# Kernel tuning notes

Hardware: AMD Instinct MI355X
Metric: run time of the kernel (lower is better)

The kernel has to match this reference:

```python
import jax, jax.numpy as jnp
import numpy as np

B, T_H, N, F_P = 16, 24, 256, 6
H, PRED_LEN, F_W = 64, 12, 4


def _build_static(coords):
    # haversine distance matrix -> gaussian kernel -> threshold (epsilon=0.5)
    lon, lat = coords[:, 0], coords[:, 1]
    dlon = lon[None, :] - lon[:, None]
    dlat = lat[None, :] - lat[:, None]
    a = (np.sin(np.radians(dlat / 2)) ** 2
         + np.cos(np.radians(lat[:, None])) * np.cos(np.radians(lat[None, :]))
         * np.sin(np.radians(dlon / 2)) ** 2)
    dist = 2.0 * 6371.0 * np.arcsin(np.sqrt(np.clip(a, 0.0, None)))
    std = dist.flatten().std()
    adj = np.exp(-np.square(dist / std))
    adj[adj < 0.5] = 0.0
    return adj.astype(np.float32)


def setup_inputs() -> dict:
    key = jax.random.key(0)
    ks = jax.random.split(key, 16)
    rng = np.random.default_rng(0)
    coords_np = np.stack([116.0 + rng.uniform(-1.0, 1.0, N),
                          40.0 + rng.uniform(-1.0, 1.0, N)], axis=1).astype(np.float32)
    s = 0.05
    scale_w = jnp.asarray([1.0, 360.0, 10.0, 1.0], jnp.float32)  # [_, dir(deg), speed, _]
    return {
        "history_pollution": jax.random.normal(ks[0], (B, T_H, N, F_P), jnp.float32),
        "history_weather": jax.random.uniform(ks[1], (B, T_H, F_W), jnp.float32) * scale_w,
        "static_adj": jnp.asarray(_build_static(coords_np)),
        "coords": jnp.asarray(coords_np),
        "w_gc1": jax.random.normal(ks[2], (H, F_P), jnp.float32) * s,
        "b_gc1": jax.random.normal(ks[3], (H,), jnp.float32) * s,
        "w_gc2": jax.random.normal(ks[4], (H, H), jnp.float32) * s,
        "b_gc2": jax.random.normal(ks[5], (H,), jnp.float32) * s,
        "w_ih": jax.random.normal(ks[6], (3 * H, H), jnp.float32) * s,
        "w_hh": jax.random.normal(ks[7], (3 * H, H), jnp.float32) * s,
        "b_ih": jax.random.normal(ks[8], (3 * H,), jnp.float32) * s,
        "b_hh": jax.random.normal(ks[9], (3 * H,), jnp.float32) * s,
        "w_m1": jax.random.normal(ks[10], (32, H), jnp.float32) * s,
        "b_m1": jax.random.normal(ks[11], (32,), jnp.float32) * s,
        "w_m2": jax.random.normal(ks[12], (F_P, 32), jnp.float32) * s,
        "b_m2": jax.random.normal(ks[13], (F_P,), jnp.float32) * s,
    }


def _forward(history_pollution, history_weather, static_adj, coords,
             w_gc1, b_gc1, w_gc2, b_gc2, w_ih, w_hh, b_ih, b_hh,
             w_m1, b_m1, w_m2, b_m2):
    Bs, Th, Ns, Fp = history_pollution.shape
    dt = history_pollution.dtype
    eye = jnp.eye(Ns, dtype=dt)
    # station pair angles: vecs[i,j] = coords[j] - coords[i]
    vecs = coords[None, :, :] - coords[:, None, :]
    ang = jnp.arctan2(vecs[..., 1], vecs[..., 0])  # [N,N]

    def gconv(x, adj, w, b):
        wt = adj + eye[None]                         # [B,N,N]
        d = 1.0 / (jnp.sqrt(wt.sum(-1)) + 1e-6)      # [B,N]
        norm = d[:, :, None] * wt * d[:, None, :]    # D^-1/2 W D^-1/2
        return jnp.einsum('bij,bjf->bif', norm, x) @ w.T + b

    def gcb(x, w_out, w_in):
        h1 = jax.nn.relu(gconv(x, w_out, w_gc1, b_gc1))
        return jax.nn.relu(gconv(h1, w_in, w_gc2, b_gc2))

    def gru(h, x):                                   # h,x: [B*N,H]
        gi = x @ w_ih.T + b_ih
        gh = h @ w_hh.T + b_hh
        i_r, i_z, i_n = jnp.split(gi, 3, axis=-1)
        h_r, h_z, h_n = jnp.split(gh, 3, axis=-1)
        r = jax.nn.sigmoid(i_r + h_r)
        z = jax.nn.sigmoid(i_z + h_z)
        n = jnp.tanh(i_n + r * h_n)
        return (1.0 - z) * n + z * h

    def mlp(x):
        return jax.nn.relu(x @ w_m1.T + b_m1) @ w_m2.T + b_m2

    def enc_step(carry, xs):
        h, _ = carry
        x_t, spd, wd = xs                            # [B,N,F],[B],[B]
        rad = jnp.deg2rad(wd)
        w_dyn = jnp.maximum(spd[:, None, None] * jnp.cos(ang[None] - rad[:, None, None]), 0.0)
        w_out = static_adj[None] * w_dyn             # [B,N,N]
        sf = gcb(x_t, w_out, jnp.swapaxes(w_out, 1, 2))
        h = gru(h, sf.reshape(Bs * Ns, -1))
        return (h, w_out), None

    h0 = jnp.zeros((Bs * Ns, w_hh.shape[1]), dt)
    xs = (jnp.moveaxis(history_pollution, 1, 0),      # [T,B,N,F]
          history_weather[:, :, 2].T,                 # wind speed [T,B]
          history_weather[:, :, 1].T)                 # wind dir   [T,B]
    (h, last_w_out), _ = jax.lax.scan(enc_step, (h0, jnp.zeros((Bs, Ns, Ns), dt)), xs)
    last_w_in = jnp.swapaxes(last_w_out, 1, 2)

    dec0 = mlp(h.reshape(Bs, Ns, -1))

    def dec_step(carry, _):
        h_c, x = carry
        sf = gcb(x, last_w_out, last_w_in)
        h_c = gru(h_c, sf.reshape(Bs * Ns, -1))
        pred = mlp(h_c.reshape(Bs, Ns, -1))
        return (h_c, pred), pred

    _, preds = jax.lax.scan(dec_step, (h, dec0), None, length=PRED_LEN)
    return jnp.moveaxis(preds, 0, 1)                  # [B, pred_len, N, F_P]


def reference(history_pollution, history_weather, static_adj, coords,
              w_gc1, b_gc1, w_gc2, b_gc2, w_ih, w_hh, b_ih, b_hh,
              w_m1, b_m1, w_m2, b_m2):
    return _forward(history_pollution, history_weather, static_adj, coords,
                    w_gc1, b_gc1, w_gc2, b_gc2, w_ih, w_hh, b_ih, b_hh,
                    w_m1, b_m1, w_m2, b_m2)
```

## Files before the change

### kernel.cpp

```cpp
#include <hip/hip_runtime.h>
#include <math.h>

#define Bsz 16
#define Tt 24
#define Nn 256
#define Fp 6
#define Hh 64
#define PredL 12
#define Fw 4
#define G3 192
#define M1 32
#define DEG2RAD 0.017453292519943295f
#define IDX2(t, b) ((t) * Bsz + (b))

__global__ __launch_bounds__(256) void k_prep_ang(
    const float* __restrict__ coords, const float* __restrict__ adj,
    float* __restrict__ Ac, float* __restrict__ As) {
  int i = blockIdx.x;
  int j = threadIdx.x;
  float dx = coords[2 * j]     - coords[2 * i];
  float dy = coords[2 * j + 1] - coords[2 * i + 1];
  float ang = atan2f(dy, dx);
  float a = adj[i * Nn + j];
  Ac[i * Nn + j] = a * cosf(ang);
  As[i * Nn + j] = a * sinf(ang);
}

__global__ __launch_bounds__(256) void k_transpose_weights(
    const float* __restrict__ wgc2, const float* __restrict__ wih,
    const float* __restrict__ whh,  const float* __restrict__ wm1,
    const float* __restrict__ wm2,
    float* __restrict__ wgc2T, float* __restrict__ wihT, float* __restrict__ whhT,
    float* __restrict__ wm1T, float* __restrict__ wm2T) {
  int tid = threadIdx.x;
  for (int idx = tid; idx < Hh * Hh; idx += 256) {
    int g = idx / Hh, k = idx % Hh;
    wgc2T[k * Hh + g] = wgc2[g * Hh + k];
  }
  for (int idx = tid; idx < G3 * Hh; idx += 256) {
    int g = idx / Hh, k = idx % Hh;
    wihT[k * G3 + g] = wih[g * Hh + k];
    whhT[k * G3 + g] = whh[g * Hh + k];
  }
  for (int idx = tid; idx < M1 * Hh; idx += 256) {
    int m = idx / Hh, k = idx % Hh;
    wm1T[k * M1 + m] = wm1[m * Hh + k];
  }
  for (int idx = tid; idx < Fp * M1; idx += 256) {
    int f = idx / M1, m = idx % M1;
    wm2T[m * Fp + f] = wm2[f * M1 + m];
  }
}

__global__ __launch_bounds__(256) void k_deg(
    const float* __restrict__ hw, const float* __restrict__ Ac,
    const float* __restrict__ As,
    float* __restrict__ dbuf, float* __restrict__ ebuf) {
  int q  = blockIdx.x & 3;
  int tb = blockIdx.x >> 2;
  int t = tb / Bsz, b = tb % Bsz;
  float spd = hw[(b * Tt + t) * Fw + 2];
  float rad = hw[(b * Tt + t) * Fw + 1] * DEG2RAD;
  float cr = cosf(rad), sr = sinf(rad);
  int w = threadIdx.x >> 6, lane = threadIdx.x & 63;
  for (int m = 0; m < 16; ++m) {
    int i = q * 64 + w * 16 + m;
    float rs = 0.f, cs = 0.f;
#pragma unroll
    for (int c = 0; c < 4; ++c) {
      int j = lane + 64 * c;
      float val = spd * (Ac[i * Nn + j] * cr + As[i * Nn + j] * sr);
      rs += fmaxf(val, 0.f);
      cs += (j == i) ? fmaxf(val, 0.f) : fmaxf(-val, 0.f);
    }
#pragma unroll
    for (int off = 32; off; off >>= 1) {
      rs += __shfl_xor(rs, off);
      cs += __shfl_xor(cs, off);
    }
    if (lane == 0) {
      dbuf[IDX2(t, b) * Nn + i] = 1.f / (sqrtf(rs + 1.f) + 1e-6f);
      ebuf[IDX2(t, b) * Nn + i] = 1.f / (sqrtf(cs + 1.f) + 1e-6f);
    }
  }
}

__global__ __launch_bounds__(256) void k_gconv1_enc(
    const float* __restrict__ hp, const float* __restrict__ hw,
    const float* __restrict__ Ac, const float* __restrict__ As,
    const float* __restrict__ dbuf,
    const float* __restrict__ wgc1, const float* __restrict__ bgc1,
    float* __restrict__ h1_all) {
  __shared__ float d_lds[Nn];
  __shared__ float x_lds[Nn * Fp];
  int ig = blockIdx.x & 15;
  int tb = blockIdx.x >> 4;
  int t = tb / Bsz, b = tb % Bsz;
  int i0 = ig * 16;
  int tid = threadIdx.x, w = tid >> 6, lane = tid & 63;
  float spd = hw[(b * Tt + t) * Fw + 2];
  float rad = hw[(b * Tt + t) * Fw + 1] * DEG2RAD;
  float cr = cosf(rad), sr = sinf(rad);
  d_lds[tid] = dbuf[IDX2(t, b) * Nn + tid];
  const float* xsrc = hp + (long)(b * Tt + t) * Nn * Fp;
#pragma unroll
  for (int c = 0; c < 6; ++c) x_lds[tid + 256 * c] = xsrc[tid + 256 * c];
  __syncthreads();
#pragma unroll
  for (int rr = 0; rr < 4; ++rr) {
    int i = i0 + w * 4 + rr;
    float acc[Fp] = {0.f, 0.f, 0.f, 0.f, 0.f, 0.f};
#pragma unroll
    for (int c = 0; c < 4; ++c) {
      int j = lane + 64 * c;
      float val = spd * (Ac[i * Nn + j] * cr + As[i * Nn + j] * sr);
      float wt = fmaxf(val, 0.f) * d_lds[j];
#pragma unroll
      for (int f = 0; f < Fp; ++f) acc[f] += wt * x_lds[j * Fp + f];
    }
#pragma unroll
    for (int f = 0; f < Fp; ++f) {
#pragma unroll
      for (int off = 32; off; off >>= 1) acc[f] += __shfl_xor(acc[f], off);
    }
    float di = d_lds[i];
    float y[Fp];
#pragma unroll
    for (int f = 0; f < Fp; ++f) y[f] = di * (acc[f] + di * x_lds[i * Fp + f]);
    float hv = bgc1[lane];
#pragma unroll
    for (int f = 0; f < Fp; ++f) hv += wgc1[lane * Fp + f] * y[f];
    h1_all[((long)IDX2(t, b) * Nn + i) * Hh + lane] = fmaxf(hv, 0.f);
  }
}

__global__ __launch_bounds__(256) void k_gconv2_enc(
    const float* __restrict__ hw, const float* __restrict__ Ac,
    const float* __restrict__ As, const float* __restrict__ ebuf,
    const float* __restrict__ h1_all,
    const float* __restrict__ wgc2T, const float* __restrict__ bgc2,
    float* __restrict__ sf_all) {
  __shared__ float e_lds[Nn];
  __shared__ __align__(16) float wvT[Nn * 20];
  __shared__ float red[4][16][Hh];
  __shared__ float y2[16][Hh];
  int ig = blockIdx.x & 15;
  int tb = blockIdx.x >> 4;
  int t = tb / Bsz, b = tb % Bsz;
  int i0 = ig * 16;
  int tid = threadIdx.x, w = tid >> 6, lane = tid & 63;
  float spd = hw[(b * Tt + t) * Fw + 2];
  float rad = hw[(b * Tt + t) * Fw + 1] * DEG2RAD;
  float cr = cosf(rad), sr = sinf(rad);
  e_lds[tid] = ebuf[IDX2(t, b) * Nn + tid];
  __syncthreads();
  float ej = e_lds[tid];
#pragma unroll
  for (int r = 0; r < 16; ++r) {
    int i = i0 + r;
    int j = tid;
    float val = spd * (Ac[i * Nn + j] * cr + As[i * Nn + j] * sr);
    float wt = (j == i) ? (fmaxf(val, 0.f) * ej + ej) : (fmaxf(-val, 0.f) * ej);
    wvT[j * 20 + r] = wt;
  }
  __syncthreads();
  float acc[16];
#pragma unroll
  for (int r = 0; r < 16; ++r) acc[r] = 0.f;
  const float* h1b = h1_all + (long)IDX2(t, b) * Nn * Hh;
#pragma unroll 4
  for (int jj = 0; jj < 64; ++jj) {
    int j = w * 64 + jj;
    float hv = h1b[j * Hh + lane];
    const float4* wp = (const float4*)(wvT + j * 20);
    float4 w0 = wp[0], w1 = wp[1], w2 = wp[2], w3 = wp[3];
    acc[0] += w0.x * hv; acc[1] += w0.y * hv; acc[2] += w0.z * hv; acc[3] += w0.w * hv;
    acc[4] += w1.x * hv; acc[5] += w1.y * hv; acc[6] += w1.z * hv; acc[7] += w1.w * hv;
    acc[8] += w2.x * hv; acc[9] += w2.y * hv; acc[10] += w2.z * hv; acc[11] += w2.w * hv;
    acc[12] += w3.x * hv; acc[13] += w3.y * hv; acc[14] += w3.z * hv; acc[15] += w3.w * hv;
  }
#pragma unroll
  for (int r = 0; r < 16; ++r) red[w][r][lane] = acc[r];
  __syncthreads();
#pragma unroll
  for (int rr = 0; rr < 4; ++rr) {
    int r = w * 4 + rr;
    float v = red[0][r][lane] + red[1][r][lane] + red[2][r][lane] + red[3][r][lane];
    y2[r][lane] = v * e_lds[i0 + r];
  }
  float a0 = bgc2[lane], a1 = a0, a2 = a0, a3 = a0;
  for (int k = 0; k < Hh; ++k) {
    float wk = wgc2T[k * Hh + lane];
    a0 += wk * y2[w * 4 + 0][k];
    a1 += wk * y2[w * 4 + 1][k];
    a2 += wk * y2[w * 4 + 2][k];
    a3 += wk * y2[w * 4 + 3][k];
  }
  long base = ((long)IDX2(t, b) * Nn + i0 + w * 4) * Hh + lane;
  sf_all[base + 0 * Hh] = fmaxf(a0, 0.f);
  sf_all[base + 1 * Hh] = fmaxf(a1, 0.f);
  sf_all[base + 2 * Hh] = fmaxf(a2, 0.f);
  sf_all[base + 3 * Hh] = fmaxf(a3, 0.f);
}

__global__ __launch_bounds__(256) void k_gru_scan(
    const float* __restrict__ sf_all,
    const float* __restrict__ wihT, const float* __restrict__ whhT,
    const float* __restrict__ bih, const float* __restrict__ bhh,
    float* __restrict__ hstate) {
  __shared__ float wih_s[Hh * G3];
  __shared__ float whh_s[Hh * G3];
  int b = blockIdx.x >> 4;
  int i0 = (blockIdx.x & 15) * 16;
  int tid = threadIdx.x, w = tid >> 6, lane = tid & 63;
  for (int idx = tid; idx < Hh * G3; idx += 256) {
    wih_s[idx] = wihT[idx];
    whh_s[idx] = whhT[idx];
  }
  __syncthreads();
  float bi_r = bih[lane], bi_z = bih[64 + lane], bi_n = bih[128 + lane];
  float bh_r = bhh[lane], bh_z = bhh[64 + lane], bh_n = bhh[128 + lane];
  float h_reg[4] = {0.f, 0.f, 0.f, 0.f};
  for (int t = 0; t < Tt; ++t) {
    float sf_reg[4];
#pragma unroll
    for (int rr = 0; rr < 4; ++rr)
      sf_reg[rr] = sf_all[((long)IDX2(t, b) * Nn + i0 + w * 4 + rr) * Hh + lane];
    float gir[4], giz[4], gin[4], ghr[4], ghz[4], ghn[4];
#pragma unroll
    for (int rr = 0; rr < 4; ++rr) {
      gir[rr] = bi_r; giz[rr] = bi_z; gin[rr] = bi_n;
      ghr[rr] = bh_r; ghz[rr] = bh_z; ghn[rr] = bh_n;
    }
#pragma unroll 4
    for (int k = 0; k < Hh; ++k) {
      float wir = wih_s[k * G3 + lane];
      float wiz = wih_s[k * G3 + 64 + lane];
      float win = wih_s[k * G3 + 128 + lane];
      float whr = whh_s[k * G3 + lane];
      float whz = whh_s[k * G3 + 64 + lane];
      float whn = whh_s[k * G3 + 128 + lane];
#pragma unroll
      for (int rr = 0; rr < 4; ++rr) {
        float sfk = __shfl(sf_reg[rr], k);
        float hk  = __shfl(h_reg[rr], k);
        gir[rr] += wir * sfk;
        giz[rr] += wiz * sfk;
        gin[rr] += win * sfk;
        ghr[rr] += whr * hk;
        ghz[rr] += whz * hk;
        ghn[rr] += whn * hk;
      }
    }
#pragma unroll
    for (int rr = 0; rr < 4; ++rr) {
      float rg = 1.f / (1.f + expf(-(gir[rr] + ghr[rr])));
      float zg = 1.f / (1.f + expf(-(giz[rr] + ghz[rr])));
      float ng = tanhf(gin[rr] + rg * ghn[rr]);
      h_reg[rr] = (1.f - zg) * ng + zg * h_reg[rr];
    }
  }
#pragma unroll
  for (int rr = 0; rr < 4; ++rr)
    hstate[((long)b * Nn + i0 + w * 4 + rr) * Hh + lane] = h_reg[rr];
}

__global__ __launch_bounds__(256) void k_norm_dec(
    const float* __restrict__ hw, const float* __restrict__ Ac,
    const float* __restrict__ As,
    const float* __restrict__ dbuf, const float* __restrict__ ebuf,
    float* __restrict__ A1d, float* __restrict__ A2d) {
  int b = blockIdx.x >> 8;
  int i = blockIdx.x & 255;
  int j = threadIdx.x;
  float spd = hw[(b * Tt + (Tt - 1)) * Fw + 2];
  float rad = hw[(b * Tt + (Tt - 1)) * Fw + 1] * DEG2RAD;
  float cr = cosf(rad), sr = sinf(rad);
  const float* drow = dbuf + IDX2(Tt - 1, b) * Nn;
  const float* erow = ebuf + IDX2(Tt - 1, b) * Nn;
  float val = spd * (Ac[i * Nn + j] * cr + As[i * Nn + j] * sr);
  float wout = fmaxf(val, 0.f);
  float win  = (j == i) ? wout : fmaxf(-val, 0.f);
  float dlt = (j == i) ? 1.f : 0.f;
  A1d[((long)b * Nn + i) * Nn + j] = drow[i] * (wout + dlt) * drow[j];
  A2d[((long)b * Nn + i) * Nn + j] = erow[i] * (win + dlt) * erow[j];
}

__global__ __launch_bounds__(256) void k_gconv1_dec(
    const float* __restrict__ xb, const float* __restrict__ A1d,
    const float* __restrict__ wgc1, const float* __restrict__ bgc1,
    float* __restrict__ h1d) {
  __shared__ float x_lds[Nn * Fp];
  int b = blockIdx.x >> 4;
  int i0 = (blockIdx.x & 15) * 16;
  int tid = threadIdx.x, w = tid >> 6, lane = tid & 63;
  const float* xsrc = xb + (long)b * Nn * Fp;
#pragma unroll
  for (int c = 0; c < 6; ++c) x_lds[tid + 256 * c] = xsrc[tid + 256 * c];
  __syncthreads();
#pragma unroll
  for (int rr = 0; rr < 4; ++rr) {
    int i = i0 + w * 4 + rr;
    const float* arow = A1d + ((long)b * Nn + i) * Nn;
    float acc[Fp] = {0.f, 0.f, 0.f, 0.f, 0.f, 0.f};
#pragma unroll
    for (int c = 0; c < 4; ++c) {
      int j = lane + 64 * c;
      float wt = arow[j];
#pragma unroll
      for (int f = 0; f < Fp; ++f) acc[f] += wt * x_lds[j * Fp + f];
    }
#pragma unroll
    for (int f = 0; f < Fp; ++f) {
#pragma unroll
      for (int off = 32; off; off >>= 1) acc[f] += __shfl_xor(acc[f], off);
    }
    float hv = bgc1[lane];
#pragma unroll
    for (int f = 0; f < Fp; ++f) hv += wgc1[lane * Fp + f] * acc[f];
    h1d[((long)b * Nn + i) * Hh + lane] = fmaxf(hv, 0.f);
  }
}

__global__ __launch_bounds__(256) void k_gconv2_gru_dec(
    const float* __restrict__ A2d, const float* __restrict__ h1d,
    const float* __restrict__ wgc2T, const float* __restrict__ bgc2,
    const float* __restrict__ wihT, const float* __restrict__ whhT,
    const float* __restrict__ bih, const float* __restrict__ bhh,
    float* __restrict__ hstate,
    const float* __restrict__ wm1T, const float* __restrict__ bm1,
    const float* __restrict__ wm2T, const float* __restrict__ bm2,
    float* __restrict__ outp, float* __restrict__ xnext, int p) {
  __shared__ __align__(16) float wvT[Nn * 20];
  __shared__ float red[4][16][Hh];
  __shared__ float y2[16][Hh];
  __shared__ float hn_lds[16][Hh];
  __shared__ float u_lds[16][M1];
  __shared__ float wih_s[Hh * G3];
  __shared__ float whh_s[Hh * G3];
  int b = blockIdx.x >> 4;
  int i0 = (blockIdx.x & 15) * 16;
  int tid = threadIdx.x, w = tid >> 6, lane = tid & 63;

  for (int idx = tid; idx < Hh * G3; idx += 256) {
    wih_s[idx] = wihT[idx];
    whh_s[idx] = whhT[idx];
  }
#pragma unroll
  for (int r = 0; r < 16; ++r)
    wvT[tid * 20 + r] = A2d[((long)b * Nn + i0 + r) * Nn + tid];
  float hp_reg[4];
#pragma unroll
  for (int rr = 0; rr < 4; ++rr)
    hp_reg[rr] = hstate[((long)b * Nn + i0 + w * 4 + rr) * Hh + lane];
  __syncthreads();

  float acc[16];
#pragma unroll
  for (int r = 0; r < 16; ++r) acc[r] = 0.f;
  const float* h1b = h1d + (long)b * Nn * Hh;
#pragma unroll 4
  for (int jj = 0; jj < 64; ++jj) {
    int j = w * 64 + jj;
    float hv = h1b[j * Hh + lane];
    const float4* wp = (const float4*)(wvT + j * 20);
    float4 w0 = wp[0], w1 = wp[1], w2 = wp[2], w3 = wp[3];
    acc[0] += w0.x * hv; acc[1] += w0.y * hv; acc[2] += w0.z * hv; acc[3] += w0.w * hv;
    acc[4] += w1.x * hv; acc[5] += w1.y * hv; acc[6] += w1.z * hv; acc[7] += w1.w * hv;
    acc[8] += w2.x * hv; acc[9] += w2.y * hv; acc[10] += w2.z * hv; acc[11] += w2.w * hv;
    acc[12] += w3.x * hv; acc[13] += w3.y * hv; acc[14] += w3.z * hv; acc[15] += w3.w * hv;
  }
#pragma unroll
  for (int r = 0; r < 16; ++r) red[w][r][lane] = acc[r];
  __syncthreads();
#pragma unroll
  for (int rr = 0; rr < 4; ++rr) {
    int r = w * 4 + rr;
    y2[r][lane] = red[0][r][lane] + red[1][r][lane] + red[2][r][lane] + red[3][r][lane];
  }
  float a0 = bgc2[lane], a1 = a0, a2 = a0, a3 = a0;
  for (int k = 0; k < Hh; ++k) {
    float wk = wgc2T[k * Hh + lane];
    a0 += wk * y2[w * 4 + 0][k];
    a1 += wk * y2[w * 4 + 1][k];
    a2 += wk * y2[w * 4 + 2][k];
    a3 += wk * y2[w * 4 + 3][k];
  }
  float sf_reg[4];
  sf_reg[0] = fmaxf(a0, 0.f);
  sf_reg[1] = fmaxf(a1, 0.f);
  sf_reg[2] = fmaxf(a2, 0.f);
  sf_reg[3] = fmaxf(a3, 0.f);

  float gir[4], giz[4], gin[4], ghr[4], ghz[4], ghn[4];
#pragma unroll
  for (int rr = 0; rr < 4; ++rr) {
    gir[rr] = bih[lane]; giz[rr] = bih[64 + lane]; gin[rr] = bih[128 + lane];
    ghr[rr] = bhh[lane]; ghz[rr] = bhh[64 + lane]; ghn[rr] = bhh[128 + lane];
  }
#pragma unroll 4
  for (int k = 0; k < Hh; ++k) {
    float wir = wih_s[k * G3 + lane];
    float wiz = wih_s[k * G3 + 64 + lane];
    float win = wih_s[k * G3 + 128 + lane];
    float whr = whh_s[k * G3 + lane];
    float whz = whh_s[k * G3 + 64 + lane];
    float whn = whh_s[k * G3 + 128 + lane];
#pragma unroll
    for (int rr = 0; rr < 4; ++rr) {
      float sfk = __shfl(sf_reg[rr], k);
      float hk  = __shfl(hp_reg[rr], k);
      gir[rr] += wir * sfk;
      giz[rr] += wiz * sfk;
      gin[rr] += win * sfk;
      ghr[rr] += whr * hk;
      ghz[rr] += whz * hk;
      ghn[rr] += whn * hk;
    }
  }
#pragma unroll
  for (int rr = 0; rr < 4; ++rr) {
    int row = w * 4 + rr;
    float rg = 1.f / (1.f + expf(-(gir[rr] + ghr[rr])));
    float zg = 1.f / (1.f + expf(-(giz[rr] + ghz[rr])));
    float ng = tanhf(gin[rr] + rg * ghn[rr]);
    float hn = (1.f - zg) * ng + zg * hp_reg[rr];
    hstate[((long)b * Nn + i0 + row) * Hh + lane] = hn;
    hn_lds[row][lane] = hn;
  }
  __syncthreads();
#pragma unroll
  for (int rep = 0; rep < 2; ++rep) {
    int idx = tid + rep * 256;
    int row = idx >> 5, m = idx & 31;
    float um = bm1[m];
    for (int k = 0; k < Hh; ++k) um += wm1T[k * M1 + m] * hn_lds[row][k];
    u_lds[row][m] = fmaxf(um, 0.f);
  }
  __syncthreads();
  if (tid < 16 * Fp) {
    int row = tid / Fp, f = tid % Fp;
    float pf = bm2[f];
#pragma unroll
    for (int m = 0; m < M1; ++m) pf += wm2T[m * Fp + f] * u_lds[row][m];
    int i = i0 + row;
    outp[(((long)b * PredL + p) * Nn + i) * Fp + f] = pf;
    xnext[((long)b * Nn + i) * Fp + f] = pf;
  }
}

__global__ __launch_bounds__(256) void k_dec0(
    const float* __restrict__ hstate,
    const float* __restrict__ wm1T, const float* __restrict__ bm1,
    const float* __restrict__ wm2T, const float* __restrict__ bm2,
    float* __restrict__ xnext) {
  const int RPB = 16;
  __shared__ float h_lds[RPB][Hh];
  __shared__ float u_lds[RPB][M1];
  int r0 = blockIdx.x * RPB;
  int tid = threadIdx.x;
#pragma unroll
  for (int c = 0; c < (RPB * Hh) / 256; ++c) {
    int idx = tid + c * 256;
    h_lds[idx >> 6][idx & 63] = hstate[(long)r0 * Hh + idx];
  }
  __syncthreads();
#pragma unroll
  for (int rep = 0; rep < 2; ++rep) {
    int idx = tid + rep * 256;
    int row = idx >> 5, m = idx & 31;
    float um = bm1[m];
    for (int k = 0; k < Hh; ++k) um += wm1T[k * M1 + m] * h_lds[row][k];
    u_lds[row][m] = fmaxf(um, 0.f);
  }
  __syncthreads();
  if (tid < RPB * Fp) {
    int row = tid / Fp, f = tid % Fp;
    float pf = bm2[f];
#pragma unroll
    for (int m = 0; m < M1; ++m) pf += wm2T[m * Fp + f] * u_lds[row][m];
    xnext[(r0 + row) * Fp + f] = pf;
  }
}

extern "C" void kernel_launch(void* const* d_in, const int* in_sizes, int n_in,
                              void* d_out, int out_size, void* d_ws, size_t ws_size,
                              hipStream_t stream) {
  const float* hp     = (const float*)d_in[0];
  const float* hw     = (const float*)d_in[1];
  const float* adj    = (const float*)d_in[2];
  const float* coords = (const float*)d_in[3];
  const float* wgc1   = (const float*)d_in[4];
  const float* bgc1   = (const float*)d_in[5];
  const float* wgc2   = (const float*)d_in[6];
  const float* bgc2   = (const float*)d_in[7];
  const float* wih    = (const float*)d_in[8];
  const float* whh    = (const float*)d_in[9];
  const float* bih    = (const float*)d_in[10];
  const float* bhh    = (const float*)d_in[11];
  const float* wm1    = (const float*)d_in[12];
  const float* bm1    = (const float*)d_in[13];
  const float* wm2    = (const float*)d_in[14];
  const float* bm2    = (const float*)d_in[15];
  float* out = (float*)d_out;

  float* w = (float*)d_ws;
  float* Ac     = w; w += Nn * Nn;
  float* As     = w; w += Nn * Nn;
  float* dbuf   = w; w += Tt * Bsz * Nn;
  float* ebuf   = w; w += Tt * Bsz * Nn;
  float* hstate = w; w += Bsz * Nn * Hh;
  float* h1_all = w; w += (long)Tt * Bsz * Nn * Hh;
  float* sf_all = w; w += (long)Tt * Bsz * Nn * Hh;
  float* h1d    = w; w += Bsz * Nn * Hh;
  float* xb     = w; w += Bsz * Nn * Fp;
  float* A1d    = w; w += Bsz * Nn * Nn;
  float* A2d    = w; w += Bsz * Nn * Nn;
  float* wgc2T  = w; w += Hh * Hh;
  float* wihT   = w; w += Hh * G3;
  float* whhT   = w; w += Hh * G3;
  float* wm1T   = w; w += Hh * M1;
  float* wm2T   = w; w += M1 * Fp;

  k_prep_ang<<<Nn, 256, 0, stream>>>(coords, adj, Ac, As);
  k_transpose_weights<<<1, 256, 0, stream>>>(wgc2, wih, whh, wm1, wm2,
                                             wgc2T, wihT, whhT, wm1T, wm2T);
  k_deg<<<Tt * Bsz * 4, 256, 0, stream>>>(hw, Ac, As, dbuf, ebuf);

  k_gconv1_enc<<<Tt * Bsz * 16, 256, 0, stream>>>(hp, hw, Ac, As, dbuf,
                                                  wgc1, bgc1, h1_all);
  k_gconv2_enc<<<Tt * Bsz * 16, 256, 0, stream>>>(hw, Ac, As, ebuf, h1_all,
                                                  wgc2T, bgc2, sf_all);
  k_gru_scan<<<Bsz * 16, 256, 0, stream>>>(sf_all, wihT, whhT, bih, bhh, hstate);

  k_norm_dec<<<Bsz * Nn, 256, 0, stream>>>(hw, Ac, As, dbuf, ebuf, A1d, A2d);
  k_dec0<<<Bsz * Nn / 16, 256, 0, stream>>>(hstate, wm1T, bm1, wm2T, bm2, xb);

  for (int p = 0; p < PredL; ++p) {
    k_gconv1_dec<<<Bsz * 16, 256, 0, stream>>>(xb, A1d, wgc1, bgc1, h1d);
    k_gconv2_gru_dec<<<Bsz * 16, 256, 0, stream>>>(
        A2d, h1d, wgc2T, bgc2, wihT, whhT, bih, bhh, hstate,
        wm1T, bm1, wm2T, bm2, out, xb, p);
  }
}
```

Baseline: 769.4 us.

## Fuse decoder steps into one kernel and repack GRU weights as float4

The two decoder kernels per prediction step become one kernel. Each block now recomputes the full first graph conv for its batch into shared memory, using a transposed adjacency matrix, and then runs gconv2, the GRU and the MLP. A ping-pong input buffer avoids a read/write race on the step's input features. The GRU weights are repacked into float4 gate triples read straight from global/L2 instead of being staged in large LDS arrays, and the encoder GRU scan uses 2 rows per wave with twice as many blocks. The trade-off is that each of the 16 blocks per batch redundantly reads the whole 256x256 adjacency and builds a 64 KB h1 tile in LDS, which may lower occupancy.

New measurement: 938.6 us. +22.0%, slower.

```diff
diff --git a/kernel.cpp b/kernel.cpp
--- a/kernel.cpp
+++ b/kernel.cpp
@@ -26,22 +26,17 @@
   As[i * Nn + j] = a * sinf(ang);
 }
 
-__global__ __launch_bounds__(256) void k_transpose_weights(
+__global__ __launch_bounds__(256) void k_prep_weights(
     const float* __restrict__ wgc2, const float* __restrict__ wih,
     const float* __restrict__ whh,  const float* __restrict__ wm1,
     const float* __restrict__ wm2,
-    float* __restrict__ wgc2T, float* __restrict__ wihT, float* __restrict__ whhT,
-    float* __restrict__ wm1T, float* __restrict__ wm2T) {
+    float* __restrict__ wgc2T, float* __restrict__ wm1T, float* __restrict__ wm2T,
+    float4* __restrict__ wihP, float4* __restrict__ whhP) {
   int tid = threadIdx.x;
   for (int idx = tid; idx < Hh * Hh; idx += 256) {
     int g = idx / Hh, k = idx % Hh;
     wgc2T[k * Hh + g] = wgc2[g * Hh + k];
   }
-  for (int idx = tid; idx < G3 * Hh; idx += 256) {
-    int g = idx / Hh, k = idx % Hh;
-    wihT[k * G3 + g] = wih[g * Hh + k];
-    whhT[k * G3 + g] = whh[g * Hh + k];
-  }
   for (int idx = tid; idx < M1 * Hh; idx += 256) {
     int m = idx / Hh, k = idx % Hh;
     wm1T[k * M1 + m] = wm1[m * Hh + k];
@@ -49,6 +44,15 @@
   for (int idx = tid; idx < Fp * M1; idx += 256) {
     int f = idx / M1, m = idx % M1;
     wm2T[m * Fp + f] = wm2[f * M1 + m];
+  }
+  for (int idx = tid; idx < Hh * 64; idx += 256) {
+    int k = idx >> 6, lane = idx & 63;
+    wihP[idx] = make_float4(wih[(0 * 64 + lane) * Hh + k],
+                            wih[(1 * 64 + lane) * Hh + k],
+                            wih[(2 * 64 + lane) * Hh + k], 0.f);
+    whhP[idx] = make_float4(whh[(0 * 64 + lane) * Hh + k],
+                            whh[(1 * 64 + lane) * Hh + k],
+                            whh[(2 * 64 + lane) * Hh + k], 0.f);
   }
 }
 
@@ -203,73 +207,74 @@
   sf_all[base + 3 * Hh] = fmaxf(a3, 0.f);
 }
 
-__global__ __launch_bounds__(256) void k_gru_scan(
+__global__ __launch_bounds__(256) void k_gru_scan3(
     const float* __restrict__ sf_all,
-    const float* __restrict__ wihT, const float* __restrict__ whhT,
+    const float4* __restrict__ wihP, const float4* __restrict__ whhP,
     const float* __restrict__ bih, const float* __restrict__ bhh,
     float* __restrict__ hstate) {
-  __shared__ float wih_s[Hh * G3];
-  __shared__ float whh_s[Hh * G3];
-  int b = blockIdx.x >> 4;
-  int i0 = (blockIdx.x & 15) * 16;
+  __shared__ float sf_s[8][Hh];
+  __shared__ float h_s[8][Hh];
+  int b = blockIdx.x >> 5;
+  int i0 = (blockIdx.x & 31) * 8;
   int tid = threadIdx.x, w = tid >> 6, lane = tid & 63;
-  for (int idx = tid; idx < Hh * G3; idx += 256) {
-    wih_s[idx] = wihT[idx];
-    whh_s[idx] = whhT[idx];
-  }
-  __syncthreads();
   float bi_r = bih[lane], bi_z = bih[64 + lane], bi_n = bih[128 + lane];
   float bh_r = bhh[lane], bh_z = bhh[64 + lane], bh_n = bhh[128 + lane];
-  float h_reg[4] = {0.f, 0.f, 0.f, 0.f};
+  float h_reg[2] = {0.f, 0.f};
+#pragma unroll
+  for (int rr = 0; rr < 2; ++rr) h_s[w * 2 + rr][lane] = 0.f;
+
   for (int t = 0; t < Tt; ++t) {
-    float sf_reg[4];
-#pragma unroll
-    for (int rr = 0; rr < 4; ++rr)
-      sf_reg[rr] = sf_all[((long)IDX2(t, b) * Nn + i0 + w * 4 + rr) * Hh + lane];
-    float gir[4], giz[4], gin[4], ghr[4], ghz[4], ghn[4];
-#pragma unroll
-    for (int rr = 0; rr < 4; ++rr) {
+#pragma unroll
+    for (int rr = 0; rr < 2; ++rr)
+      sf_s[w * 2 + rr][lane] =
+          sf_all[((long)IDX2(t, b) * Nn + i0 + w * 2 + rr) * Hh + lane];
+    float gir[2], giz[2], gin[2], ghr[2], ghz[2], ghn[2];
+#pragma unroll
+    for (int rr = 0; rr < 2; ++rr) {
       gir[rr] = bi_r; giz[rr] = bi_z; gin[rr] = bi_n;
       ghr[rr] = bh_r; ghz[rr] = bh_z; ghn[rr] = bh_n;
     }
 #pragma unroll 4
-    for (int k = 0; k < Hh; ++k) {
-      float wir = wih_s[k * G3 + lane];
-      float wiz = wih_s[k * G3 + 64 + lane];
-      float win = wih_s[k * G3 + 128 + lane];
-      float whr = whh_s[k * G3 + lane];
-      float whz = whh_s[k * G3 + 64 + lane];
-      float whn = whh_s[k * G3 + 128 + lane];
-#pragma unroll
-      for (int rr = 0; rr < 4; ++rr) {
-        float sfk = __shfl(sf_reg[rr], k);
-        float hk  = __shfl(h_reg[rr], k);
-        gir[rr] += wir * sfk;
-        giz[rr] += wiz * sfk;
-        gin[rr] += win * sfk;
-        ghr[rr] += whr * hk;
-        ghz[rr] += whz * hk;
-        ghn[rr] += whn * hk;
+    for (int kb = 0; kb < 16; ++kb) {
+      int k0 = kb * 4;
+      float4 wi[4], wh[4];
+#pragma unroll
+      for (int q = 0; q < 4; ++q) {
+        wi[q] = wihP[(k0 + q) * 64 + lane];
+        wh[q] = whhP[(k0 + q) * 64 + lane];
       }
-    }
-#pragma unroll
-    for (int rr = 0; rr < 4; ++rr) {
+#pragma unroll
+      for (int rr = 0; rr < 2; ++rr) {
+        const float4 s4 = *(const float4*)&sf_s[w * 2 + rr][k0];
+        const float4 h4 = *(const float4*)&h_s[w * 2 + rr][k0];
+        gir[rr] += s4.x * wi[0].x + s4.y * wi[1].x + s4.z * wi[2].x + s4.w * wi[3].x;
+        giz[rr] += s4.x * wi[0].y + s4.y * wi[1].y + s4.z * wi[2].y + s4.w * wi[3].y;
+        gin[rr] += s4.x * wi[0].z + s4.y * wi[1].z + s4.z * wi[2].z + s4.w * wi[3].z;
+        ghr[rr] += h4.x * wh[0].x + h4.y * wh[1].x + h4.z * wh[2].x + h4.w * wh[3].x;
+        ghz[rr] += h4.x * wh[0].y + h4.y * wh[1].y + h4.z * wh[2].y + h4.w * wh[3].y;
+        ghn[rr] += h4.x * wh[0].z + h4.y * wh[1].z + h4.z * wh[2].z + h4.w * wh[3].z;
+      }
+    }
+#pragma unroll
+    for (int rr = 0; rr < 2; ++rr) {
       float rg = 1.f / (1.f + expf(-(gir[rr] + ghr[rr])));
       float zg = 1.f / (1.f + expf(-(giz[rr] + ghz[rr])));
       float ng = tanhf(gin[rr] + rg * ghn[rr]);
-      h_reg[rr] = (1.f - zg) * ng + zg * h_reg[rr];
-    }
-  }
-#pragma unroll
-  for (int rr = 0; rr < 4; ++rr)
-    hstate[((long)b * Nn + i0 + w * 4 + rr) * Hh + lane] = h_reg[rr];
+      float hn = (1.f - zg) * ng + zg * h_reg[rr];
+      h_reg[rr] = hn;
+      h_s[w * 2 + rr][lane] = hn;
+    }
+  }
+#pragma unroll
+  for (int rr = 0; rr < 2; ++rr)
+    hstate[((long)b * Nn + i0 + w * 2 + rr) * Hh + lane] = h_reg[rr];
 }
 
 __global__ __launch_bounds__(256) void k_norm_dec(
     const float* __restrict__ hw, const float* __restrict__ Ac,
     const float* __restrict__ As,
     const float* __restrict__ dbuf, const float* __restrict__ ebuf,
-    float* __restrict__ A1d, float* __restrict__ A2d) {
+    float* __restrict__ AT, float* __restrict__ A2d) {
   int b = blockIdx.x >> 8;
   int i = blockIdx.x & 255;
   int j = threadIdx.x;
@@ -279,174 +284,10 @@
   const float* drow = dbuf + IDX2(Tt - 1, b) * Nn;
   const float* erow = ebuf + IDX2(Tt - 1, b) * Nn;
   float val = spd * (Ac[i * Nn + j] * cr + As[i * Nn + j] * sr);
-  float wout = fmaxf(val, 0.f);
-  float win  = (j == i) ? wout : fmaxf(-val, 0.f);
   float dlt = (j == i) ? 1.f : 0.f;
-  A1d[((long)b * Nn + i) * Nn + j] = drow[i] * (wout + dlt) * drow[j];
-  A2d[((long)b * Nn + i) * Nn + j] = erow[i] * (win + dlt) * erow[j];
-}
-
-__global__ __launch_bounds__(256) void k_gconv1_dec(
-    const float* __restrict__ xb, const float* __restrict__ A1d,
-    const float* __restrict__ wgc1, const float* __restrict__ bgc1,
-    float* __restrict__ h1d) {
-  __shared__ float x_lds[Nn * Fp];
-  int b = blockIdx.x >> 4;
-  int i0 = (blockIdx.x & 15) * 16;
-  int tid = threadIdx.x, w = tid >> 6, lane = tid & 63;
-  const float* xsrc = xb + (long)b * Nn * Fp;
-#pragma unroll
-  for (int c = 0; c < 6; ++c) x_lds[tid + 256 * c] = xsrc[tid + 256 * c];
-  __syncthreads();
-#pragma unroll
-  for (int rr = 0; rr < 4; ++rr) {
-    int i = i0 + w * 4 + rr;
-    const float* arow = A1d + ((long)b * Nn + i) * Nn;
-    float acc[Fp] = {0.f, 0.f, 0.f, 0.f, 0.f, 0.f};
-#pragma unroll
-    for (int c = 0; c < 4; ++c) {
-      int j = lane + 64 * c;
-      float wt = arow[j];
-#pragma unroll
-      for (int f = 0; f < Fp; ++f) acc[f] += wt * x_lds[j * Fp + f];
-    }
-#pragma unroll
-    for (int f = 0; f < Fp; ++f) {
-#pragma unroll
-      for (int off = 32; off; off >>= 1) acc[f] += __shfl_xor(acc[f], off);
-    }
-    float hv = bgc1[lane];
-#pragma unroll
-    for (int f = 0; f < Fp; ++f) hv += wgc1[lane * Fp + f] * acc[f];
-    h1d[((long)b * Nn + i) * Hh + lane] = fmaxf(hv, 0.f);
-  }
-}
-
-__global__ __launch_bounds__(256) void k_gconv2_gru_dec(
-    const float* __restrict__ A2d, const float* __restrict__ h1d,
-    const float* __restrict__ wgc2T, const float* __restrict__ bgc2,
-    const float* __restrict__ wihT, const float* __restrict__ whhT,
-    const float* __restrict__ bih, const float* __restrict__ bhh,
-    float* __restrict__ hstate,
-    const float* __restrict__ wm1T, const float* __restrict__ bm1,
-    const float* __restrict__ wm2T, const float* __restrict__ bm2,
-    float* __restrict__ outp, float* __restrict__ xnext, int p) {
-  __shared__ __align__(16) float wvT[Nn * 20];
-  __shared__ float red[4][16][Hh];
-  __shared__ float y2[16][Hh];
-  __shared__ float hn_lds[16][Hh];
-  __shared__ float u_lds[16][M1];
-  __shared__ float wih_s[Hh * G3];
-  __shared__ float whh_s[Hh * G3];
-  int b = blockIdx.x >> 4;
-  int i0 = (blockIdx.x & 15) * 16;
-  int tid = threadIdx.x, w = tid >> 6, lane = tid & 63;
-
-  for (int idx = tid; idx < Hh * G3; idx += 256) {
-    wih_s[idx] = wihT[idx];
-    whh_s[idx] = whhT[idx];
-  }
-#pragma unroll
-  for (int r = 0; r < 16; ++r)
-    wvT[tid * 20 + r] = A2d[((long)b * Nn + i0 + r) * Nn + tid];
-  float hp_reg[4];
-#pragma unroll
-  for (int rr = 0; rr < 4; ++rr)
-    hp_reg[rr] = hstate[((long)b * Nn + i0 + w * 4 + rr) * Hh + lane];
-  __syncthreads();
-
-  float acc[16];
-#pragma unroll
-  for (int r = 0; r < 16; ++r) acc[r] = 0.f;
-  const float* h1b = h1d + (long)b * Nn * Hh;
-#pragma unroll 4
-  for (int jj = 0; jj < 64; ++jj) {
-    int j = w * 64 + jj;
-    float hv = h1b[j * Hh + lane];
-    const float4* wp = (const float4*)(wvT + j * 20);
-    float4 w0 = wp[0], w1 = wp[1], w2 = wp[2], w3 = wp[3];
-    acc[0] += w0.x * hv; acc[1] += w0.y * hv; acc[2] += w0.z * hv; acc[3] += w0.w * hv;
-    acc[4] += w1.x * hv; acc[5] += w1.y * hv; acc[6] += w1.z * hv; acc[7] += w1.w * hv;
-    acc[8] += w2.x * hv; acc[9] += w2.y * hv; acc[10] += w2.z * hv; acc[11] += w2.w * hv;
-    acc[12] += w3.x * hv; acc[13] += w3.y * hv; acc[14] += w3.z * hv; acc[15] += w3.w * hv;
-  }
-#pragma unroll
-  for (int r = 0; r < 16; ++r) red[w][r][lane] = acc[r];
-  __syncthreads();
-#pragma unroll
-  for (int rr = 0; rr < 4; ++rr) {
-    int r = w * 4 + rr;
-    y2[r][lane] = red[0][r][lane] + red[1][r][lane] + red[2][r][lane] + red[3][r][lane];
-  }
-  float a0 = bgc2[lane], a1 = a0, a2 = a0, a3 = a0;
-  for (int k = 0; k < Hh; ++k) {
-    float wk = wgc2T[k * Hh + lane];
-    a0 += wk * y2[w * 4 + 0][k];
-    a1 += wk * y2[w * 4 + 1][k];
-    a2 += wk * y2[w * 4 + 2][k];
-    a3 += wk * y2[w * 4 + 3][k];
-  }
-  float sf_reg[4];
-  sf_reg[0] = fmaxf(a0, 0.f);
-  sf_reg[1] = fmaxf(a1, 0.f);
-  sf_reg[2] = fmaxf(a2, 0.f);
-  sf_reg[3] = fmaxf(a3, 0.f);
-
-  float gir[4], giz[4], gin[4], ghr[4], ghz[4], ghn[4];
-#pragma unroll
-  for (int rr = 0; rr < 4; ++rr) {
-    gir[rr] = bih[lane]; giz[rr] = bih[64 + lane]; gin[rr] = bih[128 + lane];
-    ghr[rr] = bhh[lane]; ghz[rr] = bhh[64 + lane]; ghn[rr] = bhh[128 + lane];
-  }
-#pragma unroll 4
-  for (int k = 0; k < Hh; ++k) {
-    float wir = wih_s[k * G3 + lane];
-    float wiz = wih_s[k * G3 + 64 + lane];
-    float win = wih_s[k * G3 + 128 + lane];
-    float whr = whh_s[k * G3 + lane];
-    float whz = whh_s[k * G3 + 64 + lane];
-    float whn = whh_s[k * G3 + 128 + lane];
-#pragma unroll
-    for (int rr = 0; rr < 4; ++rr) {
-      float sfk = __shfl(sf_reg[rr], k);
-      float hk  = __shfl(hp_reg[rr], k);
-      gir[rr] += wir * sfk;
-      giz[rr] += wiz * sfk;
-      gin[rr] += win * sfk;
-      ghr[rr] += whr * hk;
-      ghz[rr] += whz * hk;
-      ghn[rr] += whn * hk;
-    }
-  }
-#pragma unroll
-  for (int rr = 0; rr < 4; ++rr) {
-    int row = w * 4 + rr;
-    float rg = 1.f / (1.f + expf(-(gir[rr] + ghr[rr])));
-    float zg = 1.f / (1.f + expf(-(giz[rr] + ghz[rr])));
-    float ng = tanhf(gin[rr] + rg * ghn[rr]);
-    float hn = (1.f - zg) * ng + zg * hp_reg[rr];
-    hstate[((long)b * Nn + i0 + row) * Hh + lane] = hn;
-    hn_lds[row][lane] = hn;
-  }
-  __syncthreads();
-#pragma unroll
-  for (int rep = 0; rep < 2; ++rep) {
-    int idx = tid + rep * 256;
-    int row = idx >> 5, m = idx & 31;
-    float um = bm1[m];
-    for (int k = 0; k < Hh; ++k) um += wm1T[k * M1 + m] * hn_lds[row][k];
-    u_lds[row][m] = fmaxf(um, 0.f);
-  }
-  __syncthreads();
-  if (tid < 16 * Fp) {
-    int row = tid / Fp, f = tid % Fp;
-    float pf = bm2[f];
-#pragma unroll
-    for (int m = 0; m < M1; ++m) pf += wm2T[m * Fp + f] * u_lds[row][m];
-    int i = i0 + row;
-    outp[(((long)b * PredL + p) * Nn + i) * Fp + f] = pf;
-    xnext[((long)b * Nn + i) * Fp + f] = pf;
-  }
+  float wtji = (j == i) ? fmaxf(val, 0.f) : fmaxf(-val, 0.f);
+  AT[((long)b * Nn + i) * Nn + j]  = drow[j] * (wtji + dlt) * drow[i];
+  A2d[((long)b * Nn + i) * Nn + j] = erow[i] * (wtji + dlt) * erow[j];
 }
 
 __global__ __launch_bounds__(256) void k_dec0(
@@ -480,6 +321,179 @@
 #pragma unroll
     for (int m = 0; m < M1; ++m) pf += wm2T[m * Fp + f] * u_lds[row][m];
     xnext[(r0 + row) * Fp + f] = pf;
+  }
+}
+
+__global__ __launch_bounds__(256) void k_dec_step(
+    const float* __restrict__ AT, const float* __restrict__ A2d,
+    const float* __restrict__ xb_in, float* __restrict__ hstate,
+    const float4* __restrict__ wihP, const float4* __restrict__ whhP,
+    const float* __restrict__ wgc2T, const float* __restrict__ wgc1,
+    const float* __restrict__ bgc1, const float* __restrict__ bgc2,
+    const float* __restrict__ bih, const float* __restrict__ bhh,
+    const float* __restrict__ wm1T, const float* __restrict__ bm1,
+    const float* __restrict__ wm2T, const float* __restrict__ bm2,
+    float* __restrict__ outp, float* __restrict__ xb_out, int p) {
+  __shared__ float h1_s[Nn * Hh];
+  __shared__ __align__(16) float wvT[Nn * 20];
+  __shared__ __align__(16) float scr[4096];
+  __shared__ float y2[16][Hh];
+  __shared__ float sf_s[16][Hh];
+  __shared__ float h_s[16][Hh];
+
+  int b = blockIdx.x >> 4;
+  int i0 = (blockIdx.x & 15) * 16;
+  int tid = threadIdx.x, w = tid >> 6, lane = tid & 63;
+
+  for (int idx = tid; idx < Nn * Fp; idx += 256) {
+    int m = idx / Fp, f = idx % Fp;
+    scr[m * 8 + f] = xb_in[(long)b * Nn * Fp + idx];
+  }
+#pragma unroll
+  for (int r = 0; r < 16; ++r)
+    wvT[tid * 20 + r] = A2d[((long)b * Nn + i0 + r) * Nn + tid];
+  float hp_reg[4];
+#pragma unroll
+  for (int rr = 0; rr < 4; ++rr) {
+    hp_reg[rr] = hstate[((long)b * Nn + i0 + w * 4 + rr) * Hh + lane];
+    h_s[w * 4 + rr][lane] = hp_reg[rr];
+  }
+  float bi_r = bih[lane], bi_z = bih[64 + lane], bi_n = bih[128 + lane];
+  float bh_r = bhh[lane], bh_z = bhh[64 + lane], bh_n = bhh[128 + lane];
+  float wgc1r[Fp];
+#pragma unroll
+  for (int f = 0; f < Fp; ++f) wgc1r[f] = wgc1[lane * Fp + f];
+  float bgc1v = bgc1[lane], bgc2v = bgc2[lane];
+  __syncthreads();
+
+  {
+    float a0 = 0.f, a1 = 0.f, a2 = 0.f, a3 = 0.f, a4 = 0.f, a5 = 0.f;
+    const float* atb = AT + (long)b * Nn * Nn;
+#pragma unroll 4
+    for (int m = 0; m < Nn; ++m) {
+      float av = atb[m * Nn + tid];
+      float4 xlo = *(const float4*)&scr[m * 8];
+      float4 xhi = *(const float4*)&scr[m * 8 + 4];
+      a0 += av * xlo.x; a1 += av * xlo.y; a2 += av * xlo.z;
+      a3 += av * xlo.w; a4 += av * xhi.x; a5 += av * xhi.y;
+    }
+    __syncthreads();
+    scr[2048 + tid * 8 + 0] = a0; scr[2048 + tid * 8 + 1] = a1;
+    scr[2048 + tid * 8 + 2] = a2; scr[2048 + tid * 8 + 3] = a3;
+    scr[2048 + tid * 8 + 4] = a4; scr[2048 + tid * 8 + 5] = a5;
+  }
+  __syncthreads();
+
+#pragma unroll 4
+  for (int jj = 0; jj < 64; ++jj) {
+    int j = w * 64 + jj;
+    float4 ylo = *(const float4*)&scr[2048 + j * 8];
+    float4 yhi = *(const float4*)&scr[2048 + j * 8 + 4];
+    float hv = bgc1v + wgc1r[0] * ylo.x + wgc1r[1] * ylo.y + wgc1r[2] * ylo.z +
+               wgc1r[3] * ylo.w + wgc1r[4] * yhi.x + wgc1r[5] * yhi.y;
+    h1_s[j * Hh + lane] = fmaxf(hv, 0.f);
+  }
+  __syncthreads();
+
+  float acc[16];
+#pragma unroll
+  for (int r = 0; r < 16; ++r) acc[r] = 0.f;
+#pragma unroll 4
+  for (int jj = 0; jj < 64; ++jj) {
+    int j = w * 64 + jj;
+    float hv = h1_s[j * Hh + lane];
+    const float4* wp = (const float4*)(wvT + j * 20);
+    float4 w0 = wp[0], w1 = wp[1], w2 = wp[2], w3 = wp[3];
+    acc[0] += w0.x * hv; acc[1] += w0.y * hv; acc[2] += w0.z * hv; acc[3] += w0.w * hv;
+    acc[4] += w1.x * hv; acc[5] += w1.y * hv; acc[6] += w1.z * hv; acc[7] += w1.w * hv;
+    acc[8] += w2.x * hv; acc[9] += w2.y * hv; acc[10] += w2.z * hv; acc[11] += w2.w * hv;
+    acc[12] += w3.x * hv; acc[13] += w3.y * hv; acc[14] += w3.z * hv; acc[15] += w3.w * hv;
+  }
+  __syncthreads();
+#pragma unroll
+  for (int r = 0; r < 16; ++r) scr[w * 1024 + r * 64 + lane] = acc[r];
+  __syncthreads();
+#pragma unroll
+  for (int rr = 0; rr < 4; ++rr) {
+    int r = w * 4 + rr;
+    y2[r][lane] = scr[r * 64 + lane] + scr[1024 + r * 64 + lane] +
+                  scr[2048 + r * 64 + lane] + scr[3072 + r * 64 + lane];
+  }
+  {
+    float a0 = bgc2v, a1 = a0, a2 = a0, a3 = a0;
+    for (int k = 0; k < Hh; ++k) {
+      float wk = wgc2T[k * Hh + lane];
+      a0 += wk * y2[w * 4 + 0][k];
+      a1 += wk * y2[w * 4 + 1][k];
+      a2 += wk * y2[w * 4 + 2][k];
+      a3 += wk * y2[w * 4 + 3][k];
+    }
+    sf_s[w * 4 + 0][lane] = fmaxf(a0, 0.f);
+    sf_s[w * 4 + 1][lane] = fmaxf(a1, 0.f);
+    sf_s[w * 4 + 2][lane] = fmaxf(a2, 0.f);
+    sf_s[w * 4 + 3][lane] = fmaxf(a3, 0.f);
+  }
+
+  float hn_reg[4];
+  {
+    float gir[4], giz[4], gin[4], ghr[4], ghz[4], ghn[4];
+#pragma unroll
+    for (int rr = 0; rr < 4; ++rr) {
+      gir[rr] = bi_r; giz[rr] = bi_z; gin[rr] = bi_n;
+      ghr[rr] = bh_r; ghz[rr] = bh_z; ghn[rr] = bh_n;
+    }
+#pragma unroll 4
+    for (int kb = 0; kb < 16; ++kb) {
+      int k0 = kb * 4;
+      float4 wi[4], wh[4];
+#pragma unroll
+      for (int q = 0; q < 4; ++q) {
+        wi[q] = wihP[(k0 + q) * 64 + lane];
+        wh[q] = whhP[(k0 + q) * 64 + lane];
+      }
+#pragma unroll
+      for (int rr = 0; rr < 4; ++rr) {
+        const float4 s4 = *(const float4*)&sf_s[w * 4 + rr][k0];
+        const float4 h4 = *(const float4*)&h_s[w * 4 + rr][k0];
+        gir[rr] += s4.x * wi[0].x + s4.y * wi[1].x + s4.z * wi[2].x + s4.w * wi[3].x;
+        giz[rr] += s4.x * wi[0].y + s4.y * wi[1].y + s4.z * wi[2].y + s4.w * wi[3].y;
+        gin[rr] += s4.x * wi[0].z + s4.y * wi[1].z + s4.z * wi[2].z + s4.w * wi[3].z;
+        ghr[rr] += h4.x * wh[0].x + h4.y * wh[1].x + h4.z * wh[2].x + h4.w * wh[3].x;
+        ghz[rr] += h4.x * wh[0].y + h4.y * wh[1].y + h4.z * wh[2].y + h4.w * wh[3].y;
+        ghn[rr] += h4.x * wh[0].z + h4.y * wh[1].z + h4.z * wh[2].z + h4.w * wh[3].z;
+      }
+    }
+#pragma unroll
+    for (int rr = 0; rr < 4; ++rr) {
+      float rg = 1.f / (1.f + expf(-(gir[rr] + ghr[rr])));
+      float zg = 1.f / (1.f + expf(-(giz[rr] + ghz[rr])));
+      float ng = tanhf(gin[rr] + rg * ghn[rr]);
+      hn_reg[rr] = (1.f - zg) * ng + zg * hp_reg[rr];
+      hstate[((long)b * Nn + i0 + w * 4 + rr) * Hh + lane] = hn_reg[rr];
+    }
+  }
+
+  __syncthreads();
+#pragma unroll
+  for (int rr = 0; rr < 4; ++rr) scr[(w * 4 + rr) * 64 + lane] = hn_reg[rr];
+  __syncthreads();
+#pragma unroll
+  for (int rep = 0; rep < 2; ++rep) {
+    int idx = tid + rep * 256;
+    int row = idx >> 5, m = idx & 31;
+    float um = bm1[m];
+    for (int k = 0; k < Hh; ++k) um += wm1T[k * M1 + m] * scr[row * 64 + k];
+    scr[1024 + row * M1 + m] = fmaxf(um, 0.f);
+  }
+  __syncthreads();
+  if (tid < 16 * Fp) {
+    int row = tid / Fp, f = tid % Fp;
+    float pf = bm2[f];
+#pragma unroll
+    for (int m = 0; m < M1; ++m) pf += wm2T[m * Fp + f] * scr[1024 + row * M1 + m];
+    int i = i0 + row;
+    outp[(((long)b * PredL + p) * Nn + i) * Fp + f] = pf;
+    xb_out[((long)b * Nn + i) * Fp + f] = pf;
   }
 }
 
@@ -512,34 +526,35 @@
   float* hstate = w; w += Bsz * Nn * Hh;
   float* h1_all = w; w += (long)Tt * Bsz * Nn * Hh;
   float* sf_all = w; w += (long)Tt * Bsz * Nn * Hh;
-  float* h1d    = w; w += Bsz * Nn * Hh;
-  float* xb     = w; w += Bsz * Nn * Fp;
-  float* A1d    = w; w += Bsz * Nn * Nn;
+  float* xb0    = w; w += Bsz * Nn * Fp;
+  float* xb1    = w; w += Bsz * Nn * Fp;
+  float* AT     = w; w += Bsz * Nn * Nn;
   float* A2d    = w; w += Bsz * Nn * Nn;
   float* wgc2T  = w; w += Hh * Hh;
-  float* wihT   = w; w += Hh * G3;
-  float* whhT   = w; w += Hh * G3;
   float* wm1T   = w; w += Hh * M1;
   float* wm2T   = w; w += M1 * Fp;
+  float4* wihP  = (float4*)w; w += Hh * 64 * 4;
+  float4* whhP  = (float4*)w; w += Hh * 64 * 4;
 
   k_prep_ang<<<Nn, 256, 0, stream>>>(coords, adj, Ac, As);
-  k_transpose_weights<<<1, 256, 0, stream>>>(wgc2, wih, whh, wm1, wm2,
-                                             wgc2T, wihT, whhT, wm1T, wm2T);
+  k_prep_weights<<<1, 256, 0, stream>>>(wgc2, wih, whh, wm1, wm2,
+                                        wgc2T, wm1T, wm2T, wihP, whhP);
   k_deg<<<Tt * Bsz * 4, 256, 0, stream>>>(hw, Ac, As, dbuf, ebuf);
 
   k_gconv1_enc<<<Tt * Bsz * 16, 256, 0, stream>>>(hp, hw, Ac, As, dbuf,
                                                   wgc1, bgc1, h1_all);
   k_gconv2_enc<<<Tt * Bsz * 16, 256, 0, stream>>>(hw, Ac, As, ebuf, h1_all,
                                                   wgc2T, bgc2, sf_all);
-  k_gru_scan<<<Bsz * 16, 256, 0, stream>>>(sf_all, wihT, whhT, bih, bhh, hstate);
-
-  k_norm_dec<<<Bsz * Nn, 256, 0, stream>>>(hw, Ac, As, dbuf, ebuf, A1d, A2d);
-  k_dec0<<<Bsz * Nn / 16, 256, 0, stream>>>(hstate, wm1T, bm1, wm2T, bm2, xb);
+  k_gru_scan3<<<Bsz * 32, 256, 0, stream>>>(sf_all, wihP, whhP, bih, bhh, hstate);
+
+  k_norm_dec<<<Bsz * Nn, 256, 0, stream>>>(hw, Ac, As, dbuf, ebuf, AT, A2d);
+  k_dec0<<<Bsz * Nn / 16, 256, 0, stream>>>(hstate, wm1T, bm1, wm2T, bm2, xb0);
 
   for (int p = 0; p < PredL; ++p) {
-    k_gconv1_dec<<<Bsz * 16, 256, 0, stream>>>(xb, A1d, wgc1, bgc1, h1d);
-    k_gconv2_gru_dec<<<Bsz * 16, 256, 0, stream>>>(
-        A2d, h1d, wgc2T, bgc2, wihT, whhT, bih, bhh, hstate,
-        wm1T, bm1, wm2T, bm2, out, xb, p);
-  }
-}
+    float* xin  = (p & 1) ? xb1 : xb0;
+    float* xout = (p & 1) ? xb0 : xb1;
+    k_dec_step<<<Bsz * 16, 256, 0, stream>>>(
+        AT, A2d, xin, hstate, wihP, whhP, wgc2T, wgc1, bgc1, bgc2,
+        bih, bhh, wm1T, bm1, wm2T, bm2, out, xout, p);
+  }
+}
```
